# Kernel optimization log

Measured on AMD Instinct MI355X. Metric: run time of the kernel, lower is better.

## Reference

```python
import jax, jax.numpy as jnp
import numpy as np

LR = 0.3
AT = 0.0
DSBETA = 1e-4
EPS_DS = 1e-2

def setup_inputs() -> dict:
    key = jax.random.key(0)
    k1, k2, k3 = jax.random.split(key, 3)
    B, D, N = 65536, 256, 1024
    x = jax.random.normal(k1, (B, D), jnp.float32)
    weights = jax.random.normal(k2, (N, D), jnp.float32)
    moving_avg = jax.random.uniform(k3, (N, D), jnp.float32) * 0.1
    relevance = jnp.ones((N, D), jnp.float32)
    node_control = jnp.ones((N,), jnp.float32)
    return {"x": x, "weights": weights, "moving_avg": moving_avg,
            "relevance": relevance, "node_control": node_control}


def reference(x, weights, moving_avg, relevance, node_control):
    # SOM.forward, high-activation branch, expressed with fixed shapes:
    # per-node outputs are padded to the full [n_max, D] table and masked by
    # `has` (node received >=1 high-activation sample), which is the jit-safe
    # equivalent of torch.unique + fancy-index scatter on unique BMU ids.
    B, D = x.shape
    N = weights.shape[0]
    rel_sum = relevance.sum(axis=1)                                   # [N]
    # pairwise squared distance [B, N]
    d = ((x * x).sum(axis=1)[:, None] + (weights * weights).sum(axis=1)[None, :]
         - 2.0 * (x @ weights.T))
    dw = d * (rel_sum / D)[None, :]                                   # weighted_distance
    dw = jnp.where(jnp.isnan(dw), 0.0, dw)
    act = (rel_sum / (rel_sum + dw + 1e-7)) * node_control[None, :]   # activation * node_control
    idx = jnp.argmax(act, axis=1)                                     # BMU per sample
    act_max = jnp.max(act, axis=1)
    high = (act_max >= AT).astype(x.dtype)                            # [B]
    # unique_node_diff_vectorized: per-BMU mean of assigned high samples
    counts = jax.ops.segment_sum(high, idx, num_segments=N)           # [N]
    sums = jax.ops.segment_sum(x * high[:, None], idx, num_segments=N)  # [N, D]
    has = counts > 0
    avg_samples = sums / jnp.maximum(counts, 1.0)[:, None]            # [N, D]
    # update_node on nodes with has
    distance = jnp.abs(avg_samples - weights)
    a = LR * DSBETA
    ma_new = a * distance + (1.0 - a) * moving_avg
    ma_upd = jnp.where(has[:, None], ma_new, moving_avg)
    # NOTE: in torch, index has shape [1, n_unique] so moving_avg[index] is
    # [1, n_unique, D] and max/min/mean over dim=1 reduce ACROSS unique nodes,
    # per feature. Replicate that exactly with masked reductions over nodes.
    neg_inf = jnp.array(-jnp.inf, x.dtype)
    pos_inf = jnp.array(jnp.inf, x.dtype)
    mx = jnp.max(jnp.where(has[:, None], ma_new, neg_inf), axis=0)    # [D]
    mn = jnp.min(jnp.where(has[:, None], ma_new, pos_inf), axis=0)    # [D]
    n_has = jnp.maximum(has.sum().astype(x.dtype), 1.0)
    avg = jnp.sum(jnp.where(has[:, None], ma_new, 0.0), axis=0) / n_has  # [D]
    rel_new = 1.0 / (1.0 + jnp.exp((ma_new - avg[None, :]) / (EPS_DS * (mx - mn)[None, :])))
    rel_new = jnp.where(jnp.isnan(rel_new), 1.0, rel_new)
    rel_upd = jnp.where(has[:, None], rel_new, relevance)
    delta = jnp.where(has[:, None], LR * (avg_samples - weights), 0.0)
    w_upd = weights + delta
    loss = delta.sum() / B
    return avg_samples, w_upd, ma_upd, rel_upd, loss
```

## Files before the change

### kernel.cpp

```cpp
#include <hip/hip_runtime.h>
#include <math.h>

constexpr int DD = 256;
constexpr int NN = 1024;
constexpr float C_LR = 0.3f;
constexpr float C_DSBETA = 1e-4f;
constexpr float C_EPS_DS = 1e-2f;

using short8  = __attribute__((ext_vector_type(8))) short;
using f32x16  = __attribute__((ext_vector_type(16))) float;

__device__ __forceinline__ unsigned short f2bf(float f) {
    unsigned u = __float_as_uint(f);
    u += 0x7FFF + ((u >> 16) & 1);
    return (unsigned short)(u >> 16);
}
__device__ __forceinline__ float bf2f(unsigned short h) {
    return __uint_as_float(((unsigned)h) << 16);
}

__global__ __launch_bounds__(256) void k_init(
    const float* __restrict__ w, const float* __restrict__ rel,
    float* __restrict__ wn2, float* __restrict__ rsum, int* __restrict__ counts,
    float* __restrict__ sums,
    unsigned* __restrict__ mx_bits, unsigned* __restrict__ mn_bits,
    float* __restrict__ avgsum, int* __restrict__ n_has, float* __restrict__ loss_acc)
{
    int n = blockIdx.x, t = threadIdx.x;
    size_t o = (size_t)n * DD + t;
    float wv = w[o];
    sums[o] = 0.f;
    __shared__ float sA[256], sB[256];
    sA[t] = wv * wv; sB[t] = rel[o];
    __syncthreads();
    #pragma unroll
    for (int s = 128; s >= 1; s >>= 1) {
        if (t < s) { sA[t] += sA[t + s]; sB[t] += sB[t + s]; }
        __syncthreads();
    }
    if (t == 0) { wn2[n] = sA[0]; rsum[n] = sB[0]; counts[n] = 0; }
    if (n == 0) {
        mx_bits[t] = 0u;
        mn_bits[t] = 0x7F800000u;
        avgsum[t] = 0.f;
        if (t == 0) { *n_has = 0; *loss_acc = 0.f; }
    }
}

__global__ __launch_bounds__(256, 2) void k_main(
    const float* __restrict__ x, const float* __restrict__ wf,
    const float* __restrict__ ncontrol, const float* __restrict__ wn2,
    const float* __restrict__ rsum,
    int* __restrict__ counts, float* __restrict__ sums)
{
    __shared__ __align__(16) unsigned char smem[66560];
    __shared__ float xn2_l[64];
    __shared__ unsigned long long key_l[64][2][2];
    __shared__ int cand_l[64][2];
    __shared__ double resc[64][2];
    __shared__ int bmu_l[64];

    const int t = threadIdx.x;
    const int lane = t & 63;
    const int w = t >> 6;
    const int wm = w >> 1, wn = w & 1;
    const int m0 = wm * 32;
    const int l31 = lane & 31, half = lane >> 5;
    const int bb = blockIdx.x * 64;

    const int grow = bb + m0 + l31;
    short8 xh[16], xl[16];
    float xn2p = 0.f;
    const float* xr = x + (size_t)grow * DD + half * 8;
    #pragma unroll
    for (int s = 0; s < 16; ++s) {
        float4 a = *(const float4*)(xr + s * 16);
        float4 b = *(const float4*)(xr + s * 16 + 4);
        float f[8] = {a.x, a.y, a.z, a.w, b.x, b.y, b.z, b.w};
        #pragma unroll
        for (int j = 0; j < 8; ++j) {
            xn2p += f[j] * f[j];
            unsigned short hi = f2bf(f[j]);
            float lo = f[j] - bf2f(hi);
            xh[s][j] = (short)hi;
            xl[s][j] = (short)f2bf(lo);
        }
    }
    xn2p += __shfl_xor(xn2p, 32);
    if (wn == 0 && half == 0) xn2_l[m0 + l31] = xn2p;
    __syncthreads();

    float xn2r[16];
    #pragma unroll
    for (int r = 0; r < 16; ++r)
        xn2r[r] = xn2_l[m0 + (r & 3) + 8 * (r >> 2) + 4 * half];

    unsigned long long bestk[16], bestk2[16];
    #pragma unroll
    for (int r = 0; r < 16; ++r) { bestk[r] = 0ull; bestk2[r] = 0ull; }

    const int swz = l31 << 4;
    const int nlrow = wn * 32 + l31;
    const unsigned char* bhbase = smem + nlrow * 512;
    const unsigned char* blbase = smem + 32768 + nlrow * 512;
    const float4* wf4 = (const float4*)wf;

    for (int nt = 0; nt < 16; ++nt) {
        int ng = nt * 64 + nlrow;
        float wn2v = wn2[ng], rsv = rsum[ng], ncv = ncontrol[ng];

        #pragma unroll
        for (int p = 0; p < 16; ++p) {
            int g = p * 256 + t;
            int r = g >> 6, c = g & 63;
            float4 v = wf4[(size_t)(nt * 64 + r) * 64 + c];
            float fs[4] = {v.x, v.y, v.z, v.w};
            ushort4 hv, lv;
            unsigned short hj;
            hj = f2bf(fs[0]); hv.x = hj; lv.x = f2bf(fs[0] - bf2f(hj));
            hj = f2bf(fs[1]); hv.y = hj; lv.y = f2bf(fs[1] - bf2f(hj));
            hj = f2bf(fs[2]); hv.z = hj; lv.z = f2bf(fs[2] - bf2f(hj));
            hj = f2bf(fs[3]); hv.w = hj; lv.w = f2bf(fs[3] - bf2f(hj));
            int loff = r * 512 + ((c * 8) ^ ((r & 31) << 4));
            *(ushort4*)(smem + loff)         = hv;
            *(ushort4*)(smem + 32768 + loff) = lv;
        }
        __syncthreads();

        f32x16 acc;
        #pragma unroll
        for (int r = 0; r < 16; ++r) acc[r] = 0.f;

        #pragma unroll
        for (int s = 0; s < 16; ++s) {
            int koff = (s * 32 + half * 16) ^ swz;
            short8 bh = *(const short8*)(bhbase + koff);
            short8 bl = *(const short8*)(blbase + koff);
            acc = __builtin_amdgcn_mfma_f32_32x32x16_bf16(xh[s], bh, acc, 0, 0, 0);
            acc = __builtin_amdgcn_mfma_f32_32x32x16_bf16(xl[s], bh, acc, 0, 0, 0);
            acc = __builtin_amdgcn_mfma_f32_32x32x16_bf16(xh[s], bl, acc, 0, 0, 0);
        }

        float rvd  = rsv * (1.f / 256.f);
        float den0 = rsv + 1e-7f;
        float num  = rsv * ncv;
        unsigned inv_n = (unsigned)(NN - 1 - ng);
        #pragma unroll
        for (int r = 0; r < 16; ++r) {
            float d   = xn2r[r] + wn2v - 2.f * acc[r];
            float den = den0 + d * rvd;
            float act = num * __builtin_amdgcn_rcpf(den);
            unsigned long long key =
                ((unsigned long long)(__float_as_uint(act) | 0x80000000u) << 32) | inv_n;
            if (key > bestk[r]) { bestk2[r] = bestk[r]; bestk[r] = key; }
            else if (key > bestk2[r]) bestk2[r] = key;
        }
        __syncthreads();
    }

    #pragma unroll
    for (int mask = 1; mask <= 16; mask <<= 1) {
        #pragma unroll
        for (int r = 0; r < 16; ++r) {
            unsigned long long ob = __shfl_xor(bestk[r], mask);
            unsigned long long os = __shfl_xor(bestk2[r], mask);
            if (ob > bestk[r]) {
                bestk2[r] = (bestk[r] > os) ? bestk[r] : os;
                bestk[r]  = ob;
            } else {
                if (ob > bestk2[r]) bestk2[r] = ob;
            }
        }
    }
    if (l31 == 0) {
        #pragma unroll
        for (int r = 0; r < 16; ++r) {
            int mrow = (r & 3) + 8 * (r >> 2) + 4 * half;
            key_l[m0 + mrow][wn][0] = bestk[r];
            key_l[m0 + mrow][wn][1] = bestk2[r];
        }
    }
    __syncthreads();

    if (t < 64) {
        unsigned long long b0k = key_l[t][0][0], s0k = key_l[t][0][1];
        unsigned long long b1k = key_l[t][1][0], s1k = key_l[t][1][1];
        unsigned long long B, S;
        if (b0k > b1k) { B = b0k; S = (s0k > b1k) ? s0k : b1k; }
        else           { B = b1k; S = (s1k > b0k) ? s1k : b0k; }
        cand_l[t][0] = (NN - 1) - (int)(B & 0xFFFFFFFFull);
        cand_l[t][1] = (NN - 1) - (int)(S & 0xFFFFFFFFull);
    }
    __syncthreads();

    if (t < 128) {
        int s = t >> 1, c = t & 1;
        int node = cand_l[s][c];
        const float* xr2 = x + (size_t)(bb + s) * DD;
        const float* wr2 = wf + (size_t)node * DD;
        double a = 0.0;
        #pragma unroll 4
        for (int k = 0; k < DD; k += 4) {
            float4 xv = *(const float4*)(xr2 + k);
            float4 wv = *(const float4*)(wr2 + k);
            double d0 = (double)xv.x - (double)wv.x;
            double d1 = (double)xv.y - (double)wv.y;
            double d2 = (double)xv.z - (double)wv.z;
            double d3 = (double)xv.w - (double)wv.w;
            a += d0 * d0 + d1 * d1 + d2 * d2 + d3 * d3;
        }
        double rs = (double)rsum[node];
        double dw = a * rs * (1.0 / 256.0);
        double act = rs / (rs + dw + 1e-7) * (double)ncontrol[node];
        resc[s][c] = act;
    }
    __syncthreads();

    if (t < 64) {
        int c0 = cand_l[t][0], c1 = cand_l[t][1];
        double a0 = resc[t][0], a1 = resc[t][1];
        int bmu = c0;
        if (a1 > a0 || (a1 == a0 && c1 < c0)) bmu = c1;
        bmu_l[t] = bmu;
        atomicAdd(&counts[bmu], 1);
    }

    float* xf = (float*)smem;
    __syncthreads();
    if (wn == 0) {
        float* dst = xf + (m0 + l31) * 260 + half * 8;
        #pragma unroll
        for (int s = 0; s < 16; ++s) {
            float4 v0, v1;
            v0.x = bf2f((unsigned short)xh[s][0]) + bf2f((unsigned short)xl[s][0]);
            v0.y = bf2f((unsigned short)xh[s][1]) + bf2f((unsigned short)xl[s][1]);
            v0.z = bf2f((unsigned short)xh[s][2]) + bf2f((unsigned short)xl[s][2]);
            v0.w = bf2f((unsigned short)xh[s][3]) + bf2f((unsigned short)xl[s][3]);
            v1.x = bf2f((unsigned short)xh[s][4]) + bf2f((unsigned short)xl[s][4]);
            v1.y = bf2f((unsigned short)xh[s][5]) + bf2f((unsigned short)xl[s][5]);
            v1.z = bf2f((unsigned short)xh[s][6]) + bf2f((unsigned short)xl[s][6]);
            v1.w = bf2f((unsigned short)xh[s][7]) + bf2f((unsigned short)xl[s][7]);
            *(float4*)(dst + s * 16)     = v0;
            *(float4*)(dst + s * 16 + 4) = v1;
        }
    }
    __syncthreads();
    #pragma unroll 4
    for (int s2 = 0; s2 < 64; ++s2) {
        atomicAdd(&sums[(size_t)bmu_l[s2] * DD + t], xf[s2 * 260 + t]);
    }
}

__global__ __launch_bounds__(256) void k_node(
    const float* __restrict__ w, const float* __restrict__ ma,
    const int* __restrict__ counts, const float* __restrict__ sums,
    float* __restrict__ out_avg, float* __restrict__ out_w, float* __restrict__ out_ma,
    unsigned* __restrict__ mx_bits, unsigned* __restrict__ mn_bits,
    float* __restrict__ avgsum, int* __restrict__ n_has, float* __restrict__ loss_acc)
{
    int n = blockIdx.x, t = threadIdx.x;
    int cnt = counts[n];
    size_t o = (size_t)n * DD + t;
    bool has = cnt > 0;
    float avg = has ? sums[o] / (float)cnt : 0.f;
    float wv = w[o], mav = ma[o];
    out_avg[o] = avg;
    float dist = fabsf(avg - wv);
    const float a = C_LR * C_DSBETA;
    float man = a * dist + (1.f - a) * mav;
    out_ma[o] = has ? man : mav;
    float delta = has ? C_LR * (avg - wv) : 0.f;
    out_w[o] = wv + delta;
    if (has) {
        atomicMax(&mx_bits[t], __float_as_uint(man));
        atomicMin(&mn_bits[t], __float_as_uint(man));
        atomicAdd(&avgsum[t], man);
        if (t == 0) atomicAdd(n_has, 1);
    }
    __shared__ float rs[256];
    rs[t] = delta;
    __syncthreads();
    #pragma unroll
    for (int s2 = 128; s2 >= 1; s2 >>= 1) {
        if (t < s2) rs[t] += rs[t + s2];
        __syncthreads();
    }
    if (t == 0) atomicAdd(loss_acc, rs[0]);
}

__global__ __launch_bounds__(256) void k_rel(
    const float* __restrict__ rel_in, const float* __restrict__ out_ma,
    const int* __restrict__ counts,
    const unsigned* __restrict__ mx_bits, const unsigned* __restrict__ mn_bits,
    const float* __restrict__ avgsum, const int* __restrict__ n_has,
    const float* __restrict__ loss_acc,
    float* __restrict__ out_rel, float* __restrict__ out_loss, float invB)
{
    int n = blockIdx.x, t = threadIdx.x;
    size_t o = (size_t)n * DD + t;
    bool has = counts[n] > 0;
    float r;
    if (has) {
        float nh  = fmaxf((float)(*n_has), 1.f);
        float avg = avgsum[t] / nh;
        float mx  = __uint_as_float(mx_bits[t]);
        float mn  = __uint_as_float(mn_bits[t]);
        float man = out_ma[o];
        float targ = (man - avg) / (C_EPS_DS * (mx - mn));
        float e = expf(targ);
        float rr = 1.f / (1.f + e);
        if (!(rr == rr)) rr = 1.f;
        r = rr;
    } else {
        r = rel_in[o];
    }
    out_rel[o] = r;
    if (n == 0 && t == 0) *out_loss = (*loss_acc) * invB;
}

extern "C" void kernel_launch(void* const* d_in, const int* in_sizes, int n_in,
                              void* d_out, int out_size, void* d_ws, size_t ws_size,
                              hipStream_t stream)
{
    const float* x   = (const float*)d_in[0];
    const float* w   = (const float*)d_in[1];
    const float* ma  = (const float*)d_in[2];
    const float* rel = (const float*)d_in[3];
    const float* nc  = (const float*)d_in[4];

    const int B = in_sizes[0] / DD;
    const int ND = NN * DD;

    float* out      = (float*)d_out;
    float* out_avg  = out;
    float* out_w    = out + ND;
    float* out_ma   = out + 2 * ND;
    float* out_rel  = out + 3 * ND;
    float* out_loss = out + 4 * ND;

    char* ws = (char*)d_ws;
    size_t off = 0;
    float* sums   = (float*)(ws + off); off += (size_t)ND * 4;
    int* counts   = (int*)(ws + off); off += NN * 4;
    float* wn2    = (float*)(ws + off); off += NN * 4;
    float* rsum   = (float*)(ws + off); off += NN * 4;
    unsigned* mxb = (unsigned*)(ws + off); off += DD * 4;
    unsigned* mnb = (unsigned*)(ws + off); off += DD * 4;
    float* avgsum = (float*)(ws + off); off += DD * 4;
    int* n_has    = (int*)(ws + off); off += 256;
    float* loss_a = (float*)(ws + off); off += 256;

    k_init<<<NN, 256, 0, stream>>>(w, rel, wn2, rsum, counts, sums,
                                   mxb, mnb, avgsum, n_has, loss_a);
    k_main<<<B / 64, 256, 0, stream>>>(x, w, nc, wn2, rsum, counts, sums);
    k_node<<<NN, 256, 0, stream>>>(w, ma, counts, sums,
                                   out_avg, out_w, out_ma, mxb, mnb, avgsum, n_has, loss_a);
    k_rel<<<NN, 256, 0, stream>>>(rel, out_ma, counts, mxb, mnb, avgsum, n_has, loss_a,
                                  out_rel, out_loss, 1.0f / (float)B);
}
```

Before: 840.3 us.

## Replace per-element float atomics with BMU bucket lists and gather-sum in node kernel

Instead of every block scattering its 64 samples into a global sums table with 256 float atomicAdds each, k_main now records each sample's index in a per-node bucket with capacity 256. k_node then gathers the bucketed x rows and sums them in registers. Buckets that overflow fall back to serial per-element atomics from a single thread. This removes about 16M global float atomics, at the cost of a re-read of x in k_node, uneven work across nodes, and a very slow fallback path if BMU assignment is skewed.

```diff
diff --git a/kernel.cpp b/kernel.cpp
--- a/kernel.cpp
+++ b/kernel.cpp
@@ -3,6 +3,7 @@
 
 constexpr int DD = 256;
 constexpr int NN = 1024;
+constexpr int CAP = 256;
 constexpr float C_LR = 0.3f;
 constexpr float C_DSBETA = 1e-4f;
 constexpr float C_EPS_DS = 1e-2f;
@@ -22,14 +23,14 @@
 __global__ __launch_bounds__(256) void k_init(
     const float* __restrict__ w, const float* __restrict__ rel,
     float* __restrict__ wn2, float* __restrict__ rsum, int* __restrict__ counts,
-    float* __restrict__ sums,
+    float* __restrict__ sums_ovf,
     unsigned* __restrict__ mx_bits, unsigned* __restrict__ mn_bits,
     float* __restrict__ avgsum, int* __restrict__ n_has, float* __restrict__ loss_acc)
 {
     int n = blockIdx.x, t = threadIdx.x;
     size_t o = (size_t)n * DD + t;
     float wv = w[o];
-    sums[o] = 0.f;
+    sums_ovf[o] = 0.f;
     __shared__ float sA[256], sB[256];
     sA[t] = wv * wv; sB[t] = rel[o];
     __syncthreads();
@@ -51,14 +52,13 @@
     const float* __restrict__ x, const float* __restrict__ wf,
     const float* __restrict__ ncontrol, const float* __restrict__ wn2,
     const float* __restrict__ rsum,
-    int* __restrict__ counts, float* __restrict__ sums)
-{
-    __shared__ __align__(16) unsigned char smem[66560];
+    int* __restrict__ counts, int* __restrict__ bucket, float* __restrict__ sums_ovf)
+{
+    __shared__ __align__(16) unsigned char smem[65536];
     __shared__ float xn2_l[64];
     __shared__ unsigned long long key_l[64][2][2];
     __shared__ int cand_l[64][2];
     __shared__ double resc[64][2];
-    __shared__ int bmu_l[64];
 
     const int t = threadIdx.x;
     const int lane = t & 63;
@@ -221,48 +221,51 @@
         double a0 = resc[t][0], a1 = resc[t][1];
         int bmu = c0;
         if (a1 > a0 || (a1 == a0 && c1 < c0)) bmu = c1;
-        bmu_l[t] = bmu;
-        atomicAdd(&counts[bmu], 1);
-    }
-
-    float* xf = (float*)smem;
-    __syncthreads();
-    if (wn == 0) {
-        float* dst = xf + (m0 + l31) * 260 + half * 8;
-        #pragma unroll
-        for (int s = 0; s < 16; ++s) {
-            float4 v0, v1;
-            v0.x = bf2f((unsigned short)xh[s][0]) + bf2f((unsigned short)xl[s][0]);
-            v0.y = bf2f((unsigned short)xh[s][1]) + bf2f((unsigned short)xl[s][1]);
-            v0.z = bf2f((unsigned short)xh[s][2]) + bf2f((unsigned short)xl[s][2]);
-            v0.w = bf2f((unsigned short)xh[s][3]) + bf2f((unsigned short)xl[s][3]);
-            v1.x = bf2f((unsigned short)xh[s][4]) + bf2f((unsigned short)xl[s][4]);
-            v1.y = bf2f((unsigned short)xh[s][5]) + bf2f((unsigned short)xl[s][5]);
-            v1.z = bf2f((unsigned short)xh[s][6]) + bf2f((unsigned short)xl[s][6]);
-            v1.w = bf2f((unsigned short)xh[s][7]) + bf2f((unsigned short)xl[s][7]);
-            *(float4*)(dst + s * 16)     = v0;
-            *(float4*)(dst + s * 16 + 4) = v1;
-        }
-    }
-    __syncthreads();
-    #pragma unroll 4
-    for (int s2 = 0; s2 < 64; ++s2) {
-        atomicAdd(&sums[(size_t)bmu_l[s2] * DD + t], xf[s2 * 260 + t]);
+        int slot = atomicAdd(&counts[bmu], 1);
+        if (slot < CAP) {
+            bucket[bmu * CAP + slot] = bb + t;
+        } else {
+            const float* xrow = x + (size_t)(bb + t) * DD;
+            for (int k = 0; k < DD; ++k)
+                atomicAdd(&sums_ovf[(size_t)bmu * DD + k], xrow[k]);
+        }
     }
 }
 
 __global__ __launch_bounds__(256) void k_node(
-    const float* __restrict__ w, const float* __restrict__ ma,
-    const int* __restrict__ counts, const float* __restrict__ sums,
+    const float* __restrict__ x, const float* __restrict__ w, const float* __restrict__ ma,
+    const int* __restrict__ counts, const int* __restrict__ bucket,
+    const float* __restrict__ sums_ovf,
     float* __restrict__ out_avg, float* __restrict__ out_w, float* __restrict__ out_ma,
     unsigned* __restrict__ mx_bits, unsigned* __restrict__ mn_bits,
     float* __restrict__ avgsum, int* __restrict__ n_has, float* __restrict__ loss_acc)
 {
     int n = blockIdx.x, t = threadIdx.x;
     int cnt = counts[n];
+    int m = cnt < CAP ? cnt : CAP;
+    const int* bk = bucket + n * CAP;
+
+    float s = 0.f;
+    int j = 0;
+    for (; j + 8 <= m; j += 8) {
+        int b0 = bk[j + 0], b1 = bk[j + 1], b2 = bk[j + 2], b3 = bk[j + 3];
+        int b4 = bk[j + 4], b5 = bk[j + 5], b6 = bk[j + 6], b7 = bk[j + 7];
+        float v0 = x[(size_t)b0 * DD + t];
+        float v1 = x[(size_t)b1 * DD + t];
+        float v2 = x[(size_t)b2 * DD + t];
+        float v3 = x[(size_t)b3 * DD + t];
+        float v4 = x[(size_t)b4 * DD + t];
+        float v5 = x[(size_t)b5 * DD + t];
+        float v6 = x[(size_t)b6 * DD + t];
+        float v7 = x[(size_t)b7 * DD + t];
+        s += ((v0 + v1) + (v2 + v3)) + ((v4 + v5) + (v6 + v7));
+    }
+    for (; j < m; ++j) s += x[(size_t)bk[j] * DD + t];
+    if (cnt > CAP) s += sums_ovf[(size_t)n * DD + t];
+
+    bool has = cnt > 0;
+    float avg = has ? s / (float)cnt : 0.f;
     size_t o = (size_t)n * DD + t;
-    bool has = cnt > 0;
-    float avg = has ? sums[o] / (float)cnt : 0.f;
     float wv = w[o], mav = ma[o];
     out_avg[o] = avg;
     float dist = fabsf(avg - wv);
@@ -340,20 +343,21 @@
 
     char* ws = (char*)d_ws;
     size_t off = 0;
-    float* sums   = (float*)(ws + off); off += (size_t)ND * 4;
-    int* counts   = (int*)(ws + off); off += NN * 4;
-    float* wn2    = (float*)(ws + off); off += NN * 4;
-    float* rsum   = (float*)(ws + off); off += NN * 4;
-    unsigned* mxb = (unsigned*)(ws + off); off += DD * 4;
-    unsigned* mnb = (unsigned*)(ws + off); off += DD * 4;
-    float* avgsum = (float*)(ws + off); off += DD * 4;
-    int* n_has    = (int*)(ws + off); off += 256;
-    float* loss_a = (float*)(ws + off); off += 256;
-
-    k_init<<<NN, 256, 0, stream>>>(w, rel, wn2, rsum, counts, sums,
+    int* bucket    = (int*)(ws + off); off += (size_t)NN * CAP * 4;
+    float* sums_o  = (float*)(ws + off); off += (size_t)ND * 4;
+    int* counts    = (int*)(ws + off); off += NN * 4;
+    float* wn2     = (float*)(ws + off); off += NN * 4;
+    float* rsum    = (float*)(ws + off); off += NN * 4;
+    unsigned* mxb  = (unsigned*)(ws + off); off += DD * 4;
+    unsigned* mnb  = (unsigned*)(ws + off); off += DD * 4;
+    float* avgsum  = (float*)(ws + off); off += DD * 4;
+    int* n_has     = (int*)(ws + off); off += 256;
+    float* loss_a  = (float*)(ws + off); off += 256;
+
+    k_init<<<NN, 256, 0, stream>>>(w, rel, wn2, rsum, counts, sums_o,
                                    mxb, mnb, avgsum, n_has, loss_a);
-    k_main<<<B / 64, 256, 0, stream>>>(x, w, nc, wn2, rsum, counts, sums);
-    k_node<<<NN, 256, 0, stream>>>(w, ma, counts, sums,
+    k_main<<<B / 64, 256, 0, stream>>>(x, w, nc, wn2, rsum, counts, bucket, sums_o);
+    k_node<<<NN, 256, 0, stream>>>(x, w, ma, counts, bucket, sums_o,
                                    out_avg, out_w, out_ma, mxb, mnb, avgsum, n_has, loss_a);
     k_rel<<<NN, 256, 0, stream>>>(rel, out_ma, counts, mxb, mnb, avgsum, n_has, loss_a,
                                   out_rel, out_loss, 1.0f / (float)B);
```

Measured after the change: 1.707 ms. +103.2%, slower.
